# Performance work log

Measured on AMD Instinct MI355X. Metric: run time of the kernel, lower is better.

Reference implementation:

```python
import jax, jax.numpy as jnp
import numpy as np

B, C, N, K, G = 4, 128, 4096, 9, 4


def setup_inputs() -> dict:
    key = jax.random.key(0)
    ks = jax.random.split(key, 4)
    s = 0.05
    return {
        "features": jax.random.normal(ks[0], (B, C, N, 1), jnp.float32),
        # Attn.linear: Conv2d(2C -> C, 1x1)
        "w_lin": jax.random.normal(ks[1], (C, 2 * C), jnp.float32) * s,
        "b_lin": jnp.zeros((C,), jnp.float32),
        # atten_weight_conv: Linear(C -> K*G)
        "w_aw": jax.random.normal(ks[2], (K * G, C), jnp.float32) * s,
        "b_aw": jnp.zeros((K * G,), jnp.float32),
        # GroupNorm(4, C)
        "gn_g": jnp.ones((C,), jnp.float32),
        "gn_b": jnp.zeros((C,), jnp.float32),
        # conv: Conv2d(C -> C, 1x1) + BatchNorm2d(C)
        "conv_w": jax.random.normal(ks[3], (C, C), jnp.float32) * s,
        "conv_b": jnp.zeros((C,), jnp.float32),
        "bn_g": jnp.ones((C,), jnp.float32),
        "bn_b": jnp.zeros((C,), jnp.float32),
    }


def reference(features, w_lin, b_lin, w_aw, b_aw, gn_g, gn_b, conv_w, conv_b, bn_g, bn_b):
    B, C, N, _ = features.shape
    K, G = 9, 4
    Cg = C // G  # 32 channels per group
    EPS = 1e-5

    x = features[..., 0]                       # [B,C,N]
    # ---- KNN graph (negative squared distance, top-k) ----
    xx = jnp.sum(x * x, axis=1)                # [B,N]
    inner = jnp.einsum('bcn,bcm->bnm', x, x)   # [B,N,N]
    pd = 2.0 * inner - xx[:, :, None] - xx[:, None, :]
    idx = jax.lax.top_k(pd, K)[1]              # [B,N,K]

    # ---- edge feature gather: cat(x, x - x_neighbor) ----
    xt = x.transpose(0, 2, 1)                  # [B,N,C]
    b_ix = jnp.arange(B)[:, None, None]
    nbr = xt[b_ix, idx]                        # [B,N,K,C]
    ctr = jnp.broadcast_to(xt[:, :, None, :], (B, N, K, C))
    edge = jnp.concatenate([ctr, ctr - nbr], axis=-1)   # [B,N,K,2C]

    # ---- Attn.linear (1x1 conv == per-position linear) ----
    feat = jnp.einsum('bnke,ce->bnkc', edge, w_lin) + b_lin  # [B,N,K,C]

    # ---- grouped channel attention (4 groups of 32) ----
    fg = feat.reshape(B, N, K, G, Cg)
    scores = jnp.einsum('bnkgc,bnjgc->bngkj', fg, fg) / np.sqrt(32.0)
    s = jax.nn.softmax(scores, axis=-1)        # [B,N,G,K,K]
    attn = jnp.einsum('bngkj,bnjgc->bngkc', s, jax.nn.elu(fg))  # [B,N,G,K,Cg]

    # ---- attention weights over neighbors ----
    aw = jnp.einsum('bnc,dc->bnd', xt, w_aw) + b_aw          # [B,N,K*G]
    aw = jax.nn.softmax(aw.reshape(B, N, G, K), axis=-1)     # [B,N,G,K]

    # ---- weighted neighbor combine ----
    lf = jnp.einsum('bngk,bngkc->bngc', aw, attn)            # [B,N,G,Cg]
    lf = lf.transpose(0, 2, 3, 1).reshape(B, C, N, 1)        # [B,C,N,1]

    # ---- GroupNorm(4, C) over residual ----
    y = lf + features
    yg = y.reshape(B, G, Cg * N)
    mu = yg.mean(-1, keepdims=True)
    var = yg.var(-1, keepdims=True)
    yn = ((yg - mu) / jnp.sqrt(var + EPS)).reshape(B, C, N, 1)
    yn = yn * gn_g[None, :, None, None] + gn_b[None, :, None, None]

    # ---- 1x1 conv + BatchNorm (training-mode batch stats) + ReLU ----
    z = jnp.einsum('oc,bcnk->bonk', conv_w, yn) + conv_b[None, :, None, None]
    m = z.mean(axis=(0, 2, 3), keepdims=True)
    v = z.var(axis=(0, 2, 3), keepdims=True)
    z = (z - m) / jnp.sqrt(v + EPS) * bn_g[None, :, None, None] + bn_b[None, :, None, None]
    return jax.nn.relu(z)
```

## Files before the change

kernel.cpp:

```cpp
#include <hip/hip_runtime.h>
#include <hip/hip_bf16.h>
#include <cstddef>

#define NPTS 4096
#define CCH  128
#define KNN  9
#define GRP  4
#define BB   4
#define OFF_XT    0u
#define OFF_XX    2097152u
#define OFF_XHI   2113536u
#define OFF_IDX   3162112u
#define OFF_O     3309568u
#define OFF_Y     8159232u
#define OFF_GNP   10256384u
#define OFF_GNA   10387456u
#define OFF_GND   10387968u
#define OFF_WP    10388480u
#define OFF_BIASP 10454016u
#define OFF_BNSUM 10454528u
#define OFF_BNSQ  10454656u
#define OFF_BNSC  10454784u
#define OFF_BNSH  10454912u

using bf16x8 = __attribute__((ext_vector_type(8))) short;
using f32x4  = __attribute__((ext_vector_type(4))) float;

#define CE(a, b) { float _h = fmaxf(a, b); b = fminf(a, b); a = _h; }

#define SENT_BITS 0xFF7FF000u

__global__ void k_transpose(const float* __restrict__ x, float* __restrict__ xt,
                            __hip_bfloat16* __restrict__ xhi, float* __restrict__ xx) {
  __shared__ float t[32][33];
  int tx = threadIdx.x, ty = threadIdx.y;
  int n0 = blockIdx.x * 32, c0 = blockIdx.y * 32, b = blockIdx.z;
  float v = x[((size_t)b * CCH + c0 + ty) * NPTS + n0 + tx];
  t[ty][tx] = v;
  __syncthreads();
  float tv = t[tx][ty];
  size_t R = (size_t)b * NPTS + n0 + ty;
  int c = c0 + tx;
  xt[R * CCH + c] = tv;
  int g = c >> 3, w = c & 7;
  int sc = (((g ^ ((n0 + ty) & 15)) << 3) | w);
  xhi[R * CCH + sc] = __float2bfloat16(tv);
  if (ty == 0) {
    float s = 0.f;
    #pragma unroll
    for (int k = 0; k < 32; k++) { float u = t[k][tx]; s += u * u; }
    atomicAdd(&xx[b * NPTS + n0 + tx], s);
  }
}

__device__ __forceinline__ void select_chunk(int c, int wave, int quad,
                                             const f32x4 (&acc)[2][2],
                                             float (&top8)[2][8]) {
  const unsigned cbase = (unsigned)(c * 128 + wave * 32 + quad * 4);
  #pragma unroll
  for (int qt = 0; qt < 2; qt++) {
    float k[8];
    #pragma unroll
    for (int ct = 0; ct < 2; ct++)
      #pragma unroll
      for (int r = 0; r < 4; r++) {
        unsigned u = __float_as_uint(acc[ct][qt][r]);
        k[ct * 4 + r] = __uint_as_float((u & 0xFFFFF000u) |
                                        (cbase + (unsigned)(ct * 16 + r)));
      }
    CE(k[0],k[1]) CE(k[2],k[3]) CE(k[4],k[5]) CE(k[6],k[7])
    CE(k[0],k[2]) CE(k[1],k[3]) CE(k[4],k[6]) CE(k[5],k[7])
    CE(k[1],k[2]) CE(k[5],k[6])
    CE(k[0],k[4]) CE(k[1],k[5]) CE(k[2],k[6]) CE(k[3],k[7])
    CE(k[2],k[4]) CE(k[3],k[5])
    CE(k[1],k[2]) CE(k[3],k[4]) CE(k[5],k[6])
    float t[8];
    #pragma unroll
    for (int i = 0; i < 8; i++) t[i] = fmaxf(top8[qt][i], k[7 - i]);
    CE(t[0],t[4]) CE(t[1],t[5]) CE(t[2],t[6]) CE(t[3],t[7])
    CE(t[0],t[2]) CE(t[1],t[3]) CE(t[4],t[6]) CE(t[5],t[7])
    CE(t[0],t[1]) CE(t[2],t[3]) CE(t[4],t[5]) CE(t[6],t[7])
    #pragma unroll
    for (int i = 0; i < 8; i++) top8[qt][i] = t[i];
  }
}

__launch_bounds__(256, 3)
__global__ void k_knn(const short* __restrict__ xhi, const float* __restrict__ xx,
                      float* __restrict__ cand) {
  const int tid = threadIdx.x;
  const int wave = tid >> 6, lane = tid & 63;
  const int quad = lane >> 4, m = lane & 15;
  const int b = blockIdx.y;
  const int q0 = blockIdx.x * 32;
  const short* xb = xhi + (size_t)b * NPTS * CCH;
  const float* xxb = xx + (b << 12);

  bf16x8 qfrag[2][4];
  #pragma unroll
  for (int qt = 0; qt < 2; qt++) {
    const short* qrow = xb + (size_t)(q0 + qt * 16 + m) * CCH;
    #pragma unroll
    for (int ks = 0; ks < 4; ks++) {
      int slot = (ks * 4 + quad) ^ m;
      qfrag[qt][ks] = *(const bf16x8*)(qrow + slot * 8);
    }
  }

  int aoff[2][4];
  #pragma unroll
  for (int ct = 0; ct < 2; ct++)
    #pragma unroll
    for (int ks = 0; ks < 4; ks++)
      aoff[ct][ks] = (wave * 32 + ct * 16 + m) * CCH + (((ks * 4 + quad) ^ m) * 8);

  float top8[2][8];
  #pragma unroll
  for (int qt = 0; qt < 2; qt++)
    #pragma unroll
    for (int p = 0; p < 8; p++) top8[qt][p] = __uint_as_float(SENT_BITS);

  f32x4 acc[2][2];

  for (int c = 0; c < 32; c++) {
    bf16x8 af[2][4];
    const short* cb = xb + c * (128 * CCH);
    #pragma unroll
    for (int ct = 0; ct < 2; ct++)
      #pragma unroll
      for (int ks = 0; ks < 4; ks++)
        af[ct][ks] = *(const bf16x8*)(cb + aoff[ct][ks]);
    f32x4 cinit[2];
    #pragma unroll
    for (int ct = 0; ct < 2; ct++)
      #pragma unroll
      for (int r = 0; r < 4; r++)
        cinit[ct][r] = -0.5f * xxb[c * 128 + wave * 32 + ct * 16 + quad * 4 + r];
    if (c > 0) select_chunk(c - 1, wave, quad, acc, top8);
    #pragma unroll
    for (int ct = 0; ct < 2; ct++)
      #pragma unroll
      for (int qt = 0; qt < 2; qt++) acc[ct][qt] = cinit[ct];
    #pragma unroll
    for (int ks = 0; ks < 4; ks++)
      #pragma unroll
      for (int ct = 0; ct < 2; ct++)
        #pragma unroll
        for (int qt = 0; qt < 2; qt++)
          acc[ct][qt] = __builtin_amdgcn_mfma_f32_16x16x32_bf16(
              af[ct][ks], qfrag[qt][ks], acc[ct][qt], 0, 0, 0);
  }
  select_chunk(31, wave, quad, acc, top8);

  int slot = wave * 4 + quad;
  #pragma unroll
  for (int qt = 0; qt < 2; qt++) {
    int q = q0 + qt * 16 + m;
    float* dst = cand + ((size_t)((b << 12) + q) * 16 + slot) * 8;
    #pragma unroll
    for (int p = 0; p < 8; p++) dst[p] = top8[qt][p];
  }
}

__launch_bounds__(256)
__global__ void k_rerank(const float* __restrict__ cand, const float* __restrict__ xt,
                         const float* __restrict__ xx, int* __restrict__ idxOut) {
  __shared__ __align__(16) float arr[4][128];
  __shared__ int selS[4][16];
  __shared__ float keyS[4][16];
  int tid = threadIdx.x, wave = tid >> 6, lane = tid & 63;
  int qg = blockIdx.x * 4 + wave;
  int b = qg >> 12;
  const float* src = cand + (size_t)qg * 128;
  float e1 = src[lane], e2 = src[lane + 64];
  arr[wave][lane] = e1; arr[wave][lane + 64] = e2;
  __syncthreads();
  int r1 = 0, r2 = 0;
  #pragma unroll 8
  for (int f = 0; f < 128; f += 4) {
    float4 fv = *(const float4*)&arr[wave][f];
    r1 += (fv.x > e1) + (fv.y > e1) + (fv.z > e1) + (fv.w > e1);
    r2 += (fv.x > e2) + (fv.y > e2) + (fv.z > e2) + (fv.w > e2);
  }
  if (r1 < 16) selS[wave][r1] = (int)(__float_as_uint(e1) & 0xFFFu);
  if (r2 < 16) selS[wave][r2] = (int)(__float_as_uint(e2) & 0xFFFu);
  __syncthreads();
  int cnum = lane >> 2, part = lane & 3;
  int cidx = selS[wave][cnum];
  const float* rq = xt + (size_t)qg * CCH;
  const float* rc = xt + ((size_t)(b << 12) + cidx) * CCH;
  float dot = 0.f;
  #pragma unroll
  for (int j = 0; j < 8; j++) {
    float4 a4 = *(const float4*)&rq[part * 32 + j * 4];
    float4 c4 = *(const float4*)&rc[part * 32 + j * 4];
    dot += a4.x * c4.x + a4.y * c4.y + a4.z * c4.z + a4.w * c4.w;
  }
  dot += __shfl_xor(dot, 1);
  dot += __shfl_xor(dot, 2);
  if (part == 0)
    keyS[wave][cnum] = fmaf(2.f, dot, -xx[(b << 12) + cidx]);
  __syncthreads();
  if (lane < 16) {
    float k = keyS[wave][lane]; int i = selS[wave][lane];
    int r = 0;
    #pragma unroll
    for (int f = 0; f < 16; f++) {
      float fk = keyS[wave][f]; int fi = selS[wave][f];
      r += (fk > k) || (fk == k && fi < i);
    }
    if (r < 9) idxOut[(size_t)qg * 9 + r] = i;
  }
}

__launch_bounds__(256)
__global__ void k_linear(const float* __restrict__ xt, const float* __restrict__ w_lin,
                         const float* __restrict__ b_lin, const float* __restrict__ w_aw,
                         const float* __restrict__ b_aw, float* __restrict__ O) {
  __shared__ __align__(16) float Xs[64 * 132];
  __shared__ __align__(16) float Ws[64 * 132];
  int tid = threadIdx.x;
  int tx = tid & 15, ty = tid >> 4;
  int p0 = blockIdx.x * 64, o0 = blockIdx.y * 64;
  #pragma unroll
  for (int i = 0; i < 8; i++) {
    int flat = tid + i * 256; int r = flat >> 5, c4 = flat & 31;
    *(float4*)&Xs[r * 132 + c4 * 4] = *(const float4*)&xt[(size_t)(p0 + r) * CCH + c4 * 4];
  }
  #pragma unroll
  for (int i = 0; i < 8; i++) {
    int flat = tid + i * 256; int r = flat >> 5, c4 = flat & 31;
    int o = o0 + r; float4 v;
    if (o < 128) {
      float4 a = *(const float4*)&w_lin[(size_t)o * 256 + c4 * 4];
      float4 c = *(const float4*)&w_lin[(size_t)o * 256 + 128 + c4 * 4];
      v = make_float4(a.x + c.x, a.y + c.y, a.z + c.z, a.w + c.w);
    } else if (o < 256) {
      v = *(const float4*)&w_lin[(size_t)(o - 128) * 256 + 128 + c4 * 4];
    } else if (o < 292) {
      v = *(const float4*)&w_aw[(size_t)(o - 256) * 128 + c4 * 4];
    } else v = make_float4(0.f, 0.f, 0.f, 0.f);
    *(float4*)&Ws[r * 132 + c4 * 4] = v;
  }
  __syncthreads();
  float acc[4][4] = {};
  #pragma unroll 2
  for (int kq = 0; kq < 32; kq++) {
    float4 xa[4], wb[4];
    #pragma unroll
    for (int i = 0; i < 4; i++) xa[i] = *(const float4*)&Xs[(ty * 4 + i) * 132 + kq * 4];
    #pragma unroll
    for (int j = 0; j < 4; j++) wb[j] = *(const float4*)&Ws[(tx + 16 * j) * 132 + kq * 4];
    #pragma unroll
    for (int i = 0; i < 4; i++)
      #pragma unroll
      for (int j = 0; j < 4; j++)
        acc[i][j] += xa[i].x * wb[j].x + xa[i].y * wb[j].y + xa[i].z * wb[j].z + xa[i].w * wb[j].w;
  }
  #pragma unroll
  for (int j = 0; j < 4; j++) {
    int o = o0 + tx + 16 * j;
    if (o < 292) {
      float bias = (o < 128) ? b_lin[o] : ((o < 256) ? 0.f : b_aw[o - 256]);
      #pragma unroll
      for (int i = 0; i < 4; i++)
        O[(size_t)(p0 + ty * 4 + i) * 296 + o] = acc[i][j] + bias;
    }
  }
}

__launch_bounds__(256)
__global__ void k_attn(const float* __restrict__ O, const int* __restrict__ idxArr,
                       const float* __restrict__ xt, float* __restrict__ Y,
                       float* __restrict__ gnPart) {
  __shared__ __align__(16) float fF[4][1188];
  __shared__ __align__(16) float scS[4][432];
  __shared__ float awS[4][48];
  __shared__ float w9S[4][48];
  __shared__ int tI[45], tJ[45];
  int tid = threadIdx.x;
  int wave = tid >> 6, l = tid & 63;
  int pos = blockIdx.x * 4 + wave;
  int b = pos >> 12;
  if (tid == 0) {
    int p = 0;
    for (int i = 0; i < 9; i++) for (int j = i; j < 9; j++) { tI[p] = i; tJ[p] = j; p++; }
  }
  int nbr[9];
  const float* Op = O + (size_t)pos * 296;
  #pragma unroll
  for (int k = 0; k < 9; k++) nbr[k] = idxArr[(size_t)pos * 9 + k];
  float2 u = *(const float2*)(Op + 2 * l);
  float* fFw = fF[wave];
  #pragma unroll
  for (int k = 0; k < 9; k++) {
    const float* vp = O + (size_t)((b << 12) + nbr[k]) * 296 + 128;
    float2 vv = *(const float2*)(vp + 2 * l);
    *(float2*)&fFw[k * 132 + 2 * l] = make_float2(u.x - vv.x, u.y - vv.y);
  }
  __syncthreads();
  #pragma unroll
  for (int r = 0; r < 3; r++) {
    int p = r * 64 + l;
    if (p < 180) {
      int g = p / 45, q = p - g * 45;
      int i = tI[q], j = tJ[q];
      const float* fi = fFw + i * 132 + g * 32;
      const float* fj = fFw + j * 132 + g * 32;
      float s = 0.f;
      #pragma unroll
      for (int t8 = 0; t8 < 8; t8++) {
        float4 a4 = *(const float4*)(fi + 4 * t8);
        float4 b4 = *(const float4*)(fj + 4 * t8);
        s += a4.x * b4.x + a4.y * b4.y + a4.z * b4.z + a4.w * b4.w;
      }
      s *= 0.17677669529663687f;
      scS[wave][(g * 9 + i) * 12 + j] = s;
      scS[wave][(g * 9 + j) * 12 + i] = s;
    }
  }
  __syncthreads();
  if (l < 36) {
    int g = l / 9, i = l - g * 9;
    float* rp = &scS[wave][(g * 9 + i) * 12];
    float mx = rp[0];
    #pragma unroll
    for (int j = 1; j < 9; j++) mx = fmaxf(mx, rp[j]);
    float e[9]; float sm = 0.f;
    #pragma unroll
    for (int j = 0; j < 9; j++) { e[j] = __expf(rp[j] - mx); sm += e[j]; }
    float inv = 1.f / sm;
    #pragma unroll
    for (int j = 0; j < 9; j++) rp[j] = e[j] * inv;
  } else if (l < 40) {
    int g = l - 36;
    float a[9]; float mx = -3.4e38f;
    #pragma unroll
    for (int k = 0; k < 9; k++) { a[k] = Op[256 + g * 9 + k]; mx = fmaxf(mx, a[k]); }
    float sm = 0.f;
    #pragma unroll
    for (int k = 0; k < 9; k++) { a[k] = __expf(a[k] - mx); sm += a[k]; }
    float inv = 1.f / sm;
    #pragma unroll
    for (int k = 0; k < 9; k++) awS[wave][g * 12 + k] = a[k] * inv;
  }
  __syncthreads();
  if (l < 36) {
    int g = l / 9, j = l - g * 9;
    float s = 0.f;
    #pragma unroll
    for (int i = 0; i < 9; i++) s += awS[wave][g * 12 + i] * scS[wave][(g * 9 + i) * 12 + j];
    w9S[wave][g * 12 + j] = s;
  }
  __syncthreads();
  int g = l >> 4;
  float w9r[9];
  #pragma unroll
  for (int j = 0; j < 9; j++) w9r[j] = w9S[wave][g * 12 + j];
  int c0 = 2 * l;
  float lf0 = 0.f, lf1 = 0.f;
  #pragma unroll
  for (int j = 0; j < 9; j++) {
    float2 f2 = *(const float2*)&fFw[j * 132 + c0];
    float e0 = f2.x > 0.f ? f2.x : __expf(f2.x) - 1.f;
    float e1 = f2.y > 0.f ? f2.y : __expf(f2.y) - 1.f;
    lf0 += w9r[j] * e0;
    lf1 += w9r[j] * e1;
  }
  float2 xv = *(const float2*)(xt + (size_t)pos * CCH + c0);
  float y0 = lf0 + xv.x, y1 = lf1 + xv.y;
  *(float2*)(Y + (size_t)pos * CCH + c0) = make_float2(y0, y1);
  float s1 = y0 + y1, s2 = y0 * y0 + y1 * y1;
  #pragma unroll
  for (int mm = 1; mm <= 8; mm <<= 1) { s1 += __shfl_xor(s1, mm); s2 += __shfl_xor(s2, mm); }
  if ((l & 15) == 0) {
    gnPart[(size_t)pos * 8 + g * 2]     = s1;
    gnPart[(size_t)pos * 8 + g * 2 + 1] = s2;
  }
}

__global__ void k_gnstats(const float* __restrict__ gnPart,
                          const float* __restrict__ gn_g, const float* __restrict__ gn_b,
                          float* __restrict__ gnA, float* __restrict__ gnD) {
  int bg = blockIdx.x; int b = bg >> 2, g = bg & 3;
  int tid = threadIdx.x;
  float s1 = 0.f, s2 = 0.f;
  for (int r = tid; r < NPTS; r += 256) {
    const float* p = gnPart + (size_t)(b * NPTS + r) * 8 + g * 2;
    s1 += p[0]; s2 += p[1];
  }
  __shared__ float r1[256], r2[256];
  r1[tid] = s1; r2[tid] = s2;
  __syncthreads();
  for (int off = 128; off > 0; off >>= 1) {
    if (tid < off) { r1[tid] += r1[tid + off]; r2[tid] += r2[tid + off]; }
    __syncthreads();
  }
  __shared__ float muS, rsS;
  if (tid == 0) {
    float mu = r1[0] * (1.f / 131072.f);
    float var = r2[0] * (1.f / 131072.f) - mu * mu;
    muS = mu; rsS = 1.f / sqrtf(var + 1e-5f);
  }
  __syncthreads();
  if (tid < 32) {
    int c = g * 32 + tid;
    float a = rsS * gn_g[c];
    gnA[b * 128 + c] = a;
    gnD[b * 128 + c] = gn_b[c] - muS * a;
  }
}

__global__ void k_fold(const float* __restrict__ conv_w, const float* __restrict__ conv_b,
                       const float* __restrict__ gnA, const float* __restrict__ gnD,
                       float* __restrict__ Wp, float* __restrict__ biasp) {
  int b = blockIdx.x; int tid = threadIdx.x;
  __shared__ float dS[128], aS[128];
  if (tid < 128) { dS[tid] = gnD[b * 128 + tid]; aS[tid] = gnA[b * 128 + tid]; }
  __syncthreads();
  for (int f = tid; f < 16384; f += 256)
    Wp[(size_t)b * 16384 + f] = conv_w[f] * aS[f & 127];
  if (tid < 128) {
    float s = conv_b[tid];
    for (int c = 0; c < 128; c++) s += conv_w[tid * 128 + c] * dS[c];
    biasp[b * 128 + tid] = s;
  }
}

__launch_bounds__(256)
__global__ void k_conv(const float* __restrict__ Y, const float* __restrict__ Wp,
                       const float* __restrict__ biasp, float* __restrict__ zpre,
                       float* __restrict__ bnSum, float* __restrict__ bnSq) {
  __shared__ __align__(16) float Ys[64 * 132];
  __shared__ __align__(16) float Ws[64 * 132];
  int tid = threadIdx.x;
  int tx = tid & 15, ty = tid >> 4;
  int n0 = blockIdx.x * 64, o0 = blockIdx.y * 64, b = blockIdx.z;
  #pragma unroll
  for (int i = 0; i < 8; i++) {
    int flat = tid + i * 256; int r = flat >> 5, c4 = flat & 31;
    *(float4*)&Ys[r * 132 + c4 * 4] = *(const float4*)&Y[(size_t)((b << 12) + n0 + r) * CCH + c4 * 4];
    *(float4*)&Ws[r * 132 + c4 * 4] = *(const float4*)&Wp[(size_t)b * 16384 + (size_t)(o0 + r) * 128 + c4 * 4];
  }
  __syncthreads();
  float acc[4][4] = {};
  #pragma unroll 2
  for (int kq = 0; kq < 32; kq++) {
    float4 wa[4], yb[4];
    #pragma unroll
    for (int i = 0; i < 4; i++) wa[i] = *(const float4*)&Ws[(ty * 4 + i) * 132 + kq * 4];
    #pragma unroll
    for (int j = 0; j < 4; j++) yb[j] = *(const float4*)&Ys[(tx + 16 * j) * 132 + kq * 4];
    #pragma unroll
    for (int i = 0; i < 4; i++)
      #pragma unroll
      for (int j = 0; j < 4; j++)
        acc[i][j] += wa[i].x * yb[j].x + wa[i].y * yb[j].y + wa[i].z * yb[j].z + wa[i].w * yb[j].w;
  }
  #pragma unroll
  for (int i = 0; i < 4; i++) {
    int o = o0 + ty * 4 + i;
    float bias = biasp[b * 128 + o];
    float p1 = 0.f, p2 = 0.f;
    #pragma unroll
    for (int j = 0; j < 4; j++) {
      float z = acc[i][j] + bias;
      zpre[(((size_t)((b << 7) + o)) << 12) + n0 + tx + 16 * j] = z;
      p1 += z; p2 += z * z;
    }
    #pragma unroll
    for (int mm = 1; mm <= 8; mm <<= 1) { p1 += __shfl_xor(p1, mm); p2 += __shfl_xor(p2, mm); }
    if (tx == 0) { atomicAdd(&bnSum[o], p1); atomicAdd(&bnSq[o], p2); }
  }
}

__global__ void k_bnfin(const float* __restrict__ bnSum, const float* __restrict__ bnSq,
                        const float* __restrict__ bn_g, const float* __restrict__ bn_b,
                        float* __restrict__ bnScale, float* __restrict__ bnShift) {
  int o = threadIdx.x;
  float m = bnSum[o] * (1.f / 16384.f);
  float v = bnSq[o] * (1.f / 16384.f) - m * m;
  float sc = bn_g[o] / sqrtf(v + 1e-5f);
  bnScale[o] = sc;
  bnShift[o] = bn_b[o] - m * sc;
}

__global__ void k_final(const float* __restrict__ zpre, const float* __restrict__ bnScale,
                        const float* __restrict__ bnShift, float* __restrict__ out) {
  int i4 = blockIdx.x * 256 + threadIdx.x;
  int e = i4 * 4;
  int o = (e >> 12) & 127;
  float4 z = *(const float4*)&zpre[e];
  float sc = bnScale[o], sh = bnShift[o];
  float4 r;
  r.x = fmaxf(fmaf(z.x, sc, sh), 0.f);
  r.y = fmaxf(fmaf(z.y, sc, sh), 0.f);
  r.z = fmaxf(fmaf(z.z, sc, sh), 0.f);
  r.w = fmaxf(fmaf(z.w, sc, sh), 0.f);
  *(float4*)&out[e] = r;
}

extern "C" void kernel_launch(void* const* d_in, const int* in_sizes, int n_in,
                              void* d_out, int out_size, void* d_ws, size_t ws_size,
                              hipStream_t stream) {
  const float* features = (const float*)d_in[0];
  const float* w_lin  = (const float*)d_in[1];
  const float* b_lin  = (const float*)d_in[2];
  const float* w_aw   = (const float*)d_in[3];
  const float* b_aw   = (const float*)d_in[4];
  const float* gn_g   = (const float*)d_in[5];
  const float* gn_b   = (const float*)d_in[6];
  const float* conv_w = (const float*)d_in[7];
  const float* conv_b = (const float*)d_in[8];
  const float* bn_g   = (const float*)d_in[9];
  const float* bn_b   = (const float*)d_in[10];

  float* ws    = (float*)d_ws;
  float* xt    = ws + OFF_XT;
  float* xxp   = ws + OFF_XX;
  __hip_bfloat16* xhip = (__hip_bfloat16*)(ws + OFF_XHI);
  int*   idxp  = (int*)(ws + OFF_IDX);
  float* Op    = ws + OFF_O;
  float* candp = ws + OFF_O;
  float* Yp    = ws + OFF_Y;
  float* gnp   = ws + OFF_GNP;
  float* gnA   = ws + OFF_GNA;
  float* gnD   = ws + OFF_GND;
  float* Wp    = ws + OFF_WP;
  float* biasp = ws + OFF_BIASP;
  float* bnSum = ws + OFF_BNSUM;
  float* bnSq  = ws + OFF_BNSQ;
  float* bnSc  = ws + OFF_BNSC;
  float* bnSh  = ws + OFF_BNSH;
  float* zpre  = xt;

  hipMemsetAsync(xxp, 0, NPTS * BB * sizeof(float), stream);
  hipMemsetAsync(bnSum, 0, 256 * sizeof(float), stream);

  k_transpose<<<dim3(128, 4, 4), dim3(32, 32), 0, stream>>>(features, xt, xhip, xxp);
  k_knn<<<dim3(128, 4), 256, 0, stream>>>((const short*)xhip, xxp, candp);
  k_rerank<<<4096, 256, 0, stream>>>(candp, xt, xxp, idxp);
  k_linear<<<dim3(256, 5), 256, 0, stream>>>(xt, w_lin, b_lin, w_aw, b_aw, Op);
  k_attn<<<4096, 256, 0, stream>>>(Op, idxp, xt, Yp, gnp);
  k_gnstats<<<16, 256, 0, stream>>>(gnp, gn_g, gn_b, gnA, gnD);
  k_fold<<<4, 256, 0, stream>>>(conv_w, conv_b, gnA, gnD, Wp, biasp);
  k_conv<<<dim3(64, 2, 4), 256, 0, stream>>>(Yp, Wp, biasp, zpre, bnSum, bnSq);
  k_bnfin<<<1, 128, 0, stream>>>(bnSum, bnSq, bn_g, bn_b, bnSc, bnSh);
  k_final<<<2048, 256, 0, stream>>>(zpre, bnSc, bnSh, (float*)d_out);
}
```

Measured before the change: 295.6 us.

## Double-buffer candidate chunk loads in KNN kernel with ping-pong registers

```diff
diff --git a/kernel.cpp b/kernel.cpp
--- a/kernel.cpp
+++ b/kernel.cpp
@@ -85,7 +85,44 @@
   }
 }
 
-__launch_bounds__(256, 3)
+__device__ __forceinline__ void load_chunk(const short* __restrict__ xb,
+                                           const int (&aoff)[2][4], int c,
+                                           bf16x8 (&af)[2][4]) {
+  const short* cb = xb + c * (128 * CCH);
+  #pragma unroll
+  for (int ct = 0; ct < 2; ct++)
+    #pragma unroll
+    for (int ks = 0; ks < 4; ks++)
+      af[ct][ks] = *(const bf16x8*)(cb + aoff[ct][ks]);
+}
+
+__device__ __forceinline__ void load_cinit(const float* __restrict__ xxb, int base, int c,
+                                           f32x4 (&ci)[2]) {
+  #pragma unroll
+  for (int ct = 0; ct < 2; ct++)
+    #pragma unroll
+    for (int r = 0; r < 4; r++)
+      ci[ct][r] = -0.5f * xxb[c * 128 + base + ct * 16 + r];
+}
+
+__device__ __forceinline__ void mfma_chunk(const bf16x8 (&af)[2][4],
+                                           const bf16x8 (&qf)[2][4],
+                                           const f32x4 (&ci)[2], f32x4 (&acc)[2][2]) {
+  #pragma unroll
+  for (int ct = 0; ct < 2; ct++)
+    #pragma unroll
+    for (int qt = 0; qt < 2; qt++) acc[ct][qt] = ci[ct];
+  #pragma unroll
+  for (int ks = 0; ks < 4; ks++)
+    #pragma unroll
+    for (int ct = 0; ct < 2; ct++)
+      #pragma unroll
+      for (int qt = 0; qt < 2; qt++)
+        acc[ct][qt] = __builtin_amdgcn_mfma_f32_16x16x32_bf16(
+            af[ct][ks], qf[qt][ks], acc[ct][qt], 0, 0, 0);
+}
+
+__launch_bounds__(256, 2)
 __global__ void k_knn(const short* __restrict__ xhi, const float* __restrict__ xx,
                       float* __restrict__ cand) {
   const int tid = threadIdx.x;
@@ -95,6 +132,7 @@
   const int q0 = blockIdx.x * 32;
   const short* xb = xhi + (size_t)b * NPTS * CCH;
   const float* xxb = xx + (b << 12);
+  const int base = wave * 32 + quad * 4;
 
   bf16x8 qfrag[2][4];
   #pragma unroll
@@ -121,34 +159,23 @@
     for (int p = 0; p < 8; p++) top8[qt][p] = __uint_as_float(SENT_BITS);
 
   f32x4 acc[2][2];
-
-  for (int c = 0; c < 32; c++) {
-    bf16x8 af[2][4];
-    const short* cb = xb + c * (128 * CCH);
-    #pragma unroll
-    for (int ct = 0; ct < 2; ct++)
-      #pragma unroll
-      for (int ks = 0; ks < 4; ks++)
-        af[ct][ks] = *(const bf16x8*)(cb + aoff[ct][ks]);
-    f32x4 cinit[2];
-    #pragma unroll
-    for (int ct = 0; ct < 2; ct++)
-      #pragma unroll
-      for (int r = 0; r < 4; r++)
-        cinit[ct][r] = -0.5f * xxb[c * 128 + wave * 32 + ct * 16 + quad * 4 + r];
+  bf16x8 bufA[2][4], bufB[2][4];
+  f32x4 ciA[2], ciB[2];
+
+  load_chunk(xb, aoff, 0, bufA);
+  load_cinit(xxb, base, 0, ciA);
+
+  for (int c = 0; c < 32; c += 2) {
+    load_chunk(xb, aoff, c + 1, bufB);
+    load_cinit(xxb, base, c + 1, ciB);
     if (c > 0) select_chunk(c - 1, wave, quad, acc, top8);
-    #pragma unroll
-    for (int ct = 0; ct < 2; ct++)
-      #pragma unroll
-      for (int qt = 0; qt < 2; qt++) acc[ct][qt] = cinit[ct];
-    #pragma unroll
-    for (int ks = 0; ks < 4; ks++)
-      #pragma unroll
-      for (int ct = 0; ct < 2; ct++)
-        #pragma unroll
-        for (int qt = 0; qt < 2; qt++)
-          acc[ct][qt] = __builtin_amdgcn_mfma_f32_16x16x32_bf16(
-              af[ct][ks], qfrag[qt][ks], acc[ct][qt], 0, 0, 0);
+    mfma_chunk(bufA, qfrag, ciA, acc);
+    if (c + 2 < 32) {
+      load_chunk(xb, aoff, c + 2, bufA);
+      load_cinit(xxb, base, c + 2, ciA);
+    }
+    select_chunk(c, wave, quad, acc, top8);
+    mfma_chunk(bufB, qfrag, ciB, acc);
   }
   select_chunk(31, wave, quad, acc, top8);
 
```

Result: faster. 275.5 us (-6.8%).
